# Kernel tuning notes

Measured on AMD Instinct MI355X. Metric: run time of the kernel, lower is better.

Reference implementation:

```python
import jax, jax.numpy as jnp
import numpy as np

N = 8_000_000
NUM_MOLS = 200_000

def setup_inputs() -> dict:
    key = jax.random.key(0)
    k1, k2 = jax.random.split(key)
    atoms_x = jax.random.normal(k1, (N, 3), dtype=jnp.float32)
    graph_batch = jnp.sort(jax.random.randint(k2, (N,), 0, NUM_MOLS, dtype=jnp.int64))
    return {"atoms_x": atoms_x, "graph_batch": graph_batch, "num_mols": NUM_MOLS}

def reference(atoms_x, graph_batch, num_mols):
    # Per-molecule mean via single-pass segment reduction (replaces O(N*num_mols) mask loop)
    seg_sum = jax.ops.segment_sum(atoms_x, graph_batch, num_segments=num_mols)          # [M, 3]
    counts = jax.ops.segment_sum(jnp.ones((atoms_x.shape[0],), atoms_x.dtype),
                                 graph_batch, num_segments=num_mols)                    # [M]
    mean = seg_sum / jnp.maximum(counts, 1.0)[:, None]                                  # empty mols -> 0 center
    return atoms_x - mean[graph_batch]
```

## Files before the change

kernel.cpp:

```cpp
#include <hip/hip_runtime.h>


static constexpr int WAVE   = 64;
static constexpr int WPB    = 4;
static constexpr int TPB    = WAVE * WPB;
static constexpr int CPT    = 16;
static constexpr int WCHUNK = WAVE * CPT;
static constexpr int BCHUNK = WCHUNK * WPB;
static constexpr int SLOTS  = 128;

#define LDS_FENCE() asm volatile("s_waitcnt lgkmcnt(0)" ::: "memory")

__global__ __launch_bounds__(TPB) void fused_center_kernel(
    const float* __restrict__ x, const int* __restrict__ gb,
    float* __restrict__ out, int n) {
  __shared__ float sums_all[WPB][SLOTS * 4];

  const int w = threadIdx.x >> 6;
  const int lane = threadIdx.x & 63;
  float* sums = sums_all[w];

  const long long cs = (long long)blockIdx.x * BCHUNK + (long long)w * WCHUNK;
  if (cs >= (long long)n) return;
  const long long ce = (cs + WCHUNK < (long long)n) ? cs + WCHUNK : (long long)n;
  const int fid = gb[cs];
  const int lid = gb[ce - 1];
  const int span = lid - fid + 1;

  if (span > SLOTS) {
    if (lane == 0) {
      long long i = cs;
      while (i < ce) {
        int id = gb[i];
        long long rs = i; while (rs > 0 && gb[rs - 1] == id) --rs;
        long long re = i; while (re < n && gb[re] == id) ++re;
        float sx = 0.f, sy = 0.f, sz = 0.f;
        for (long long k = rs; k < re; ++k) {
          sx += x[k * 3 + 0]; sy += x[k * 3 + 1]; sz += x[k * 3 + 2];
        }
        float inv = 1.f / (float)(re - rs);
        float mx = sx * inv, my = sy * inv, mz = sz * inv;
        long long we = (re < ce) ? re : ce;
        for (long long k = i; k < we; ++k) {
          out[k * 3 + 0] = x[k * 3 + 0] - mx;
          out[k * 3 + 1] = x[k * 3 + 1] - my;
          out[k * 3 + 2] = x[k * 3 + 2] - mz;
        }
        i = we;
      }
    }
    return;
  }

  const long long base = cs + (long long)lane * CPT;
  const bool full = (base + CPT <= ce);

  float f[CPT * 3];
  int ids[CPT];
  if (full) {
    const float4* xv = reinterpret_cast<const float4*>(x + base * 3);
#pragma unroll
    for (int j = 0; j < CPT * 3 / 4; ++j) {
      float4 v = xv[j];
      f[j * 4 + 0] = v.x; f[j * 4 + 1] = v.y;
      f[j * 4 + 2] = v.z; f[j * 4 + 3] = v.w;
    }
    const int4* gv = reinterpret_cast<const int4*>(gb + base);
#pragma unroll
    for (int j = 0; j < CPT / 4; ++j) {
      int4 g = gv[j];
      ids[j * 4 + 0] = g.x; ids[j * 4 + 1] = g.y;
      ids[j * 4 + 2] = g.z; ids[j * 4 + 3] = g.w;
    }
  }

  for (int i = lane; i < span * 4; i += WAVE) sums[i] = 0.f;
  LDS_FENCE();

  if (full) {
    int cur = ids[0];
    float sx = 0.f, sy = 0.f, sz = 0.f, sc = 0.f;
#pragma unroll
    for (int j = 0; j < CPT; ++j) {
      if (ids[j] != cur) {
        int s = (cur - fid) * 4;
        atomicAdd(&sums[s + 0], sx); atomicAdd(&sums[s + 1], sy);
        atomicAdd(&sums[s + 2], sz); atomicAdd(&sums[s + 3], sc);
        cur = ids[j]; sx = sy = sz = sc = 0.f;
      }
      sx += f[j * 3 + 0]; sy += f[j * 3 + 1]; sz += f[j * 3 + 2]; sc += 1.f;
    }
    {
      int s = (cur - fid) * 4;
      atomicAdd(&sums[s + 0], sx); atomicAdd(&sums[s + 1], sy);
      atomicAdd(&sums[s + 2], sz); atomicAdd(&sums[s + 3], sc);
    }
  } else if (base < ce) {
    for (long long i = base; i < ce; ++i) {
      int s = (gb[i] - fid) * 4;
      atomicAdd(&sums[s + 0], x[i * 3 + 0]);
      atomicAdd(&sums[s + 1], x[i * 3 + 1]);
      atomicAdd(&sums[s + 2], x[i * 3 + 2]);
      atomicAdd(&sums[s + 3], 1.f);
    }
  }

  if (cs > 0) {
    float hx = 0.f, hy = 0.f, hz = 0.f, hc = 0.f;
    long long off = 1 + lane;
    for (;;) {
      long long i = cs - off;
      bool m = (i >= 0) && (gb[i] == fid);
      if (m) {
        hx += x[i * 3 + 0]; hy += x[i * 3 + 1]; hz += x[i * 3 + 2]; hc += 1.f;
      }
      if (__popcll(__ballot(m)) < WAVE) break;
      off += WAVE;
    }
#pragma unroll
    for (int d = 1; d < 64; d <<= 1) {
      hx += __shfl_xor(hx, d); hy += __shfl_xor(hy, d);
      hz += __shfl_xor(hz, d); hc += __shfl_xor(hc, d);
    }
    if (lane == 0 && hc > 0.f) {
      atomicAdd(&sums[0], hx); atomicAdd(&sums[1], hy);
      atomicAdd(&sums[2], hz); atomicAdd(&sums[3], hc);
    }
  }
  if (ce < (long long)n) {
    float hx = 0.f, hy = 0.f, hz = 0.f, hc = 0.f;
    long long off = (long long)lane;
    for (;;) {
      long long i = ce + off;
      bool m = (i < (long long)n) && (gb[i] == lid);
      if (m) {
        hx += x[i * 3 + 0]; hy += x[i * 3 + 1]; hz += x[i * 3 + 2]; hc += 1.f;
      }
      if (__popcll(__ballot(m)) < WAVE) break;
      off += WAVE;
    }
#pragma unroll
    for (int d = 1; d < 64; d <<= 1) {
      hx += __shfl_xor(hx, d); hy += __shfl_xor(hy, d);
      hz += __shfl_xor(hz, d); hc += __shfl_xor(hc, d);
    }
    if (lane == 0 && hc > 0.f) {
      int s = (lid - fid) * 4;
      atomicAdd(&sums[s + 0], hx); atomicAdd(&sums[s + 1], hy);
      atomicAdd(&sums[s + 2], hz); atomicAdd(&sums[s + 3], hc);
    }
  }
  LDS_FENCE();

  for (int s = lane; s < span; s += WAVE) {
    float c = sums[s * 4 + 3];
    if (c > 0.f) {
      float inv = 1.f / c;
      sums[s * 4 + 0] *= inv; sums[s * 4 + 1] *= inv; sums[s * 4 + 2] *= inv;
    }
  }
  LDS_FENCE();

  if (full) {
#pragma unroll
    for (int j = 0; j < CPT; ++j) {
      int s = (ids[j] - fid) * 4;
      f[j * 3 + 0] -= sums[s + 0];
      f[j * 3 + 1] -= sums[s + 1];
      f[j * 3 + 2] -= sums[s + 2];
    }
    float4* ov = reinterpret_cast<float4*>(out + base * 3);
#pragma unroll
    for (int j = 0; j < CPT * 3 / 4; ++j)
      ov[j] = make_float4(f[j * 4 + 0], f[j * 4 + 1],
                          f[j * 4 + 2], f[j * 4 + 3]);
  } else if (base < ce) {
    for (long long i = base; i < ce; ++i) {
      int s = (gb[i] - fid) * 4;
      out[i * 3 + 0] = x[i * 3 + 0] - sums[s + 0];
      out[i * 3 + 1] = x[i * 3 + 1] - sums[s + 1];
      out[i * 3 + 2] = x[i * 3 + 2] - sums[s + 2];
    }
  }
}

extern "C" void kernel_launch(void* const* d_in, const int* in_sizes, int n_in,
                              void* d_out, int out_size, void* d_ws, size_t ws_size,
                              hipStream_t stream) {
  const float* x = (const float*)d_in[0];
  const int* gb = (const int*)d_in[1];
  float* out = (float*)d_out;
  const int n = in_sizes[0] / 3;

  int blocks = (int)(((long long)n + BCHUNK - 1) / BCHUNK);
  fused_center_kernel<<<blocks, TPB, 0, stream>>>(x, gb, out, n);
}
```

Before: 53.22 us.

## Process two chunks per wave with both chunks' loads issued up front

Each wave now handles two consecutive chunks of 12 atoms per lane. It issues the global loads for both chunks before processing the first, so memory latency for the second chunk overlaps with the first chunk's reduction and write-back. Other changes: fid/lid come from register shuffles instead of extra global loads, LDS is zeroed with float4 stores across fixed slots, and the slot count shrinks to 96. The cost is higher register pressure from the two 48-float buffers, which could lower occupancy.

New measurement: 61.47 us. +15.5%, slower.

```diff
diff --git a/kernel.cpp b/kernel.cpp
--- a/kernel.cpp
+++ b/kernel.cpp
@@ -4,27 +4,56 @@
 static constexpr int WAVE   = 64;
 static constexpr int WPB    = 4;
 static constexpr int TPB    = WAVE * WPB;
-static constexpr int CPT    = 16;
+static constexpr int CPT    = 12;
 static constexpr int WCHUNK = WAVE * CPT;
-static constexpr int BCHUNK = WCHUNK * WPB;
-static constexpr int SLOTS  = 128;
+static constexpr int ITERS  = 2;
+static constexpr int SLOTS  = 96;
 
 #define LDS_FENCE() asm volatile("s_waitcnt lgkmcnt(0)" ::: "memory")
 
-__global__ __launch_bounds__(TPB) void fused_center_kernel(
+__device__ __forceinline__ void issue_loads(
     const float* __restrict__ x, const int* __restrict__ gb,
-    float* __restrict__ out, int n) {
-  __shared__ float sums_all[WPB][SLOTS * 4];
-
-  const int w = threadIdx.x >> 6;
-  const int lane = threadIdx.x & 63;
-  float* sums = sums_all[w];
-
-  const long long cs = (long long)blockIdx.x * BCHUNK + (long long)w * WCHUNK;
-  if (cs >= (long long)n) return;
-  const long long ce = (cs + WCHUNK < (long long)n) ? cs + WCHUNK : (long long)n;
-  const int fid = gb[cs];
-  const int lid = gb[ce - 1];
+    long long cs, long long ce, int lane,
+    float* f, int* ids, bool& full) {
+  long long base = cs + (long long)lane * CPT;
+  full = (base + CPT <= ce);
+  if (full) {
+    const float4* xv = reinterpret_cast<const float4*>(x + base * 3);
+#pragma unroll
+    for (int j = 0; j < CPT * 3 / 4; ++j) {
+      float4 v = xv[j];
+      f[j * 4 + 0] = v.x; f[j * 4 + 1] = v.y;
+      f[j * 4 + 2] = v.z; f[j * 4 + 3] = v.w;
+    }
+    const int4* gv = reinterpret_cast<const int4*>(gb + base);
+#pragma unroll
+    for (int j = 0; j < CPT / 4; ++j) {
+      int4 g = gv[j];
+      ids[j * 4 + 0] = g.x; ids[j * 4 + 1] = g.y;
+      ids[j * 4 + 2] = g.z; ids[j * 4 + 3] = g.w;
+    }
+  }
+}
+
+__device__ __forceinline__ void process_chunk(
+    const float* __restrict__ x, const int* __restrict__ gb,
+    float* __restrict__ out, int n, long long cs, long long ce,
+    int lane, float* __restrict__ sums,
+    float* f, int* ids, bool full) {
+  LDS_FENCE();
+  {
+    float4* s4 = reinterpret_cast<float4*>(sums);
+    float4 z = make_float4(0.f, 0.f, 0.f, 0.f);
+#pragma unroll
+    for (int i = 0; i < (SLOTS + WAVE - 1) / WAVE; ++i) {
+      int s = i * WAVE + lane;
+      if (s < SLOTS) s4[s] = z;
+    }
+  }
+
+  const bool partial = (ce - cs) < WCHUNK;
+  const int fid = partial ? gb[cs] : __shfl(ids[0], 0);
+  const int lid = partial ? gb[ce - 1] : __shfl(ids[CPT - 1], WAVE - 1);
   const int span = lid - fid + 1;
 
   if (span > SLOTS) {
@@ -53,29 +82,6 @@
   }
 
   const long long base = cs + (long long)lane * CPT;
-  const bool full = (base + CPT <= ce);
-
-  float f[CPT * 3];
-  int ids[CPT];
-  if (full) {
-    const float4* xv = reinterpret_cast<const float4*>(x + base * 3);
-#pragma unroll
-    for (int j = 0; j < CPT * 3 / 4; ++j) {
-      float4 v = xv[j];
-      f[j * 4 + 0] = v.x; f[j * 4 + 1] = v.y;
-      f[j * 4 + 2] = v.z; f[j * 4 + 3] = v.w;
-    }
-    const int4* gv = reinterpret_cast<const int4*>(gb + base);
-#pragma unroll
-    for (int j = 0; j < CPT / 4; ++j) {
-      int4 g = gv[j];
-      ids[j * 4 + 0] = g.x; ids[j * 4 + 1] = g.y;
-      ids[j * 4 + 2] = g.z; ids[j * 4 + 3] = g.w;
-    }
-  }
-
-  for (int i = lane; i < span * 4; i += WAVE) sums[i] = 0.f;
-  LDS_FENCE();
 
   if (full) {
     int cur = ids[0];
@@ -184,6 +190,37 @@
   }
 }
 
+__global__ __launch_bounds__(TPB) void fused_center_kernel(
+    const float* __restrict__ x, const int* __restrict__ gb,
+    float* __restrict__ out, int n, int nchunks) {
+  __shared__ float sums_all[WPB][SLOTS * 4];
+
+  const int w = threadIdx.x >> 6;
+  const int lane = threadIdx.x & 63;
+  float* sums = sums_all[w];
+
+  const long long g = (long long)blockIdx.x * WPB + w;
+  const long long c0 = g * ITERS;
+  const long long c1 = c0 + 1;
+  if (c0 >= nchunks) return;
+
+  const long long cs0 = c0 * WCHUNK;
+  const long long ce0 = (cs0 + WCHUNK < (long long)n) ? cs0 + WCHUNK : (long long)n;
+  const bool hasB = (c1 < nchunks);
+  const long long cs1 = c1 * WCHUNK;
+  const long long ce1 = (cs1 + WCHUNK < (long long)n) ? cs1 + WCHUNK : (long long)n;
+
+  float fA[CPT * 3]; int idsA[CPT]; bool fullA = false;
+  float fB[CPT * 3]; int idsB[CPT]; bool fullB = false;
+
+  issue_loads(x, gb, cs0, ce0, lane, fA, idsA, fullA);
+  if (hasB) issue_loads(x, gb, cs1, ce1, lane, fB, idsB, fullB);
+
+  process_chunk(x, gb, out, n, cs0, ce0, lane, sums, fA, idsA, fullA);
+  if (hasB)
+    process_chunk(x, gb, out, n, cs1, ce1, lane, sums, fB, idsB, fullB);
+}
+
 extern "C" void kernel_launch(void* const* d_in, const int* in_sizes, int n_in,
                               void* d_out, int out_size, void* d_ws, size_t ws_size,
                               hipStream_t stream) {
@@ -192,6 +229,8 @@
   float* out = (float*)d_out;
   const int n = in_sizes[0] / 3;
 
-  int blocks = (int)(((long long)n + BCHUNK - 1) / BCHUNK);
-  fused_center_kernel<<<blocks, TPB, 0, stream>>>(x, gb, out, n);
-}
+  int nchunks = (int)(((long long)n + WCHUNK - 1) / WCHUNK);
+  long long nwaves = (nchunks + ITERS - 1) / ITERS;
+  int blocks = (int)((nwaves + WPB - 1) / WPB);
+  fused_center_kernel<<<blocks, TPB, 0, stream>>>(x, gb, out, n, nchunks);
+}
```

## Coalesce global loads through padded LDS staging with single-wave blocks

Applied to the files above, without the earlier changes.

Switches each lane from loading its own contiguous strided chunk to coalesced float4/int4 loads across the wave. The data is staged in padded LDS buffers so each lane can then read its own 8 consecutive atoms for segmented accumulation. The output is written back coalesced, with each element's molecule id found by a multiply-shift divide-by-3. Blocks shrink to one wave with 8 atoms per thread and fewer LDS slots, and the tail chunk and fallback are split into separate paths. The aim is better memory coalescing and occupancy, at the cost of extra LDS traffic and index math.

Result: slower. 60.97 us (+14.6%).

```diff
diff --git a/kernel.cpp b/kernel.cpp
--- a/kernel.cpp
+++ b/kernel.cpp
@@ -2,107 +2,172 @@
 
 
 static constexpr int WAVE   = 64;
-static constexpr int WPB    = 4;
-static constexpr int TPB    = WAVE * WPB;
-static constexpr int CPT    = 16;
+static constexpr int TPB    = 64;
+static constexpr int CPT    = 8;
 static constexpr int WCHUNK = WAVE * CPT;
-static constexpr int BCHUNK = WCHUNK * WPB;
-static constexpr int SLOTS  = 128;
+static constexpr int SLOTS  = 96;
+static constexpr int NGRP   = WCHUNK / 16;
+static constexpr int XGRP   = 216;
+static constexpr int IGRP   = 72;
 
 #define LDS_FENCE() asm volatile("s_waitcnt lgkmcnt(0)" ::: "memory")
+
+__device__ void serial_fallback(const float* __restrict__ x,
+                                const int* __restrict__ gb,
+                                float* __restrict__ out, int n,
+                                long long cs, long long ce, int lane) {
+  if (lane != 0) return;
+  long long i = cs;
+  while (i < ce) {
+    int id = gb[i];
+    long long rs = i; while (rs > 0 && gb[rs - 1] == id) --rs;
+    long long re = i; while (re < n && gb[re] == id) ++re;
+    float sx = 0.f, sy = 0.f, sz = 0.f;
+    for (long long k = rs; k < re; ++k) {
+      sx += x[k * 3 + 0]; sy += x[k * 3 + 1]; sz += x[k * 3 + 2];
+    }
+    float inv = 1.f / (float)(re - rs);
+    float mx = sx * inv, my = sy * inv, mz = sz * inv;
+    long long we = (re < ce) ? re : ce;
+    for (long long k = i; k < we; ++k) {
+      out[k * 3 + 0] = x[k * 3 + 0] - mx;
+      out[k * 3 + 1] = x[k * 3 + 1] - my;
+      out[k * 3 + 2] = x[k * 3 + 2] - mz;
+    }
+    i = we;
+  }
+}
 
 __global__ __launch_bounds__(TPB) void fused_center_kernel(
     const float* __restrict__ x, const int* __restrict__ gb,
     float* __restrict__ out, int n) {
-  __shared__ float sums_all[WPB][SLOTS * 4];
-
-  const int w = threadIdx.x >> 6;
-  const int lane = threadIdx.x & 63;
-  float* sums = sums_all[w];
-
-  const long long cs = (long long)blockIdx.x * BCHUNK + (long long)w * WCHUNK;
-  if (cs >= (long long)n) return;
+  __shared__ alignas(16) char xbuf[NGRP * XGRP];
+  __shared__ alignas(16) char ibuf[NGRP * IGRP];
+  __shared__ alignas(16) float sums[SLOTS * 4];
+
+  const int lane = threadIdx.x;
+  const long long cs = (long long)blockIdx.x * WCHUNK;
   const long long ce = (cs + WCHUNK < (long long)n) ? cs + WCHUNK : (long long)n;
-  const int fid = gb[cs];
-  const int lid = gb[ce - 1];
-  const int span = lid - fid + 1;
-
-  if (span > SLOTS) {
-    if (lane == 0) {
-      long long i = cs;
-      while (i < ce) {
-        int id = gb[i];
-        long long rs = i; while (rs > 0 && gb[rs - 1] == id) --rs;
-        long long re = i; while (re < n && gb[re] == id) ++re;
-        float sx = 0.f, sy = 0.f, sz = 0.f;
-        for (long long k = rs; k < re; ++k) {
-          sx += x[k * 3 + 0]; sy += x[k * 3 + 1]; sz += x[k * 3 + 2];
-        }
-        float inv = 1.f / (float)(re - rs);
-        float mx = sx * inv, my = sy * inv, mz = sz * inv;
-        long long we = (re < ce) ? re : ce;
-        for (long long k = i; k < we; ++k) {
-          out[k * 3 + 0] = x[k * 3 + 0] - mx;
-          out[k * 3 + 1] = x[k * 3 + 1] - my;
-          out[k * 3 + 2] = x[k * 3 + 2] - mz;
-        }
-        i = we;
-      }
-    }
-    return;
-  }
-
-  const long long base = cs + (long long)lane * CPT;
-  const bool full = (base + CPT <= ce);
-
-  float f[CPT * 3];
-  int ids[CPT];
-  if (full) {
-    const float4* xv = reinterpret_cast<const float4*>(x + base * 3);
-#pragma unroll
-    for (int j = 0; j < CPT * 3 / 4; ++j) {
-      float4 v = xv[j];
-      f[j * 4 + 0] = v.x; f[j * 4 + 1] = v.y;
-      f[j * 4 + 2] = v.z; f[j * 4 + 3] = v.w;
-    }
-    const int4* gv = reinterpret_cast<const int4*>(gb + base);
-#pragma unroll
-    for (int j = 0; j < CPT / 4; ++j) {
-      int4 g = gv[j];
-      ids[j * 4 + 0] = g.x; ids[j * 4 + 1] = g.y;
-      ids[j * 4 + 2] = g.z; ids[j * 4 + 3] = g.w;
-    }
-  }
-
-  for (int i = lane; i < span * 4; i += WAVE) sums[i] = 0.f;
-  LDS_FENCE();
-
-  if (full) {
-    int cur = ids[0];
-    float sx = 0.f, sy = 0.f, sz = 0.f, sc = 0.f;
-#pragma unroll
-    for (int j = 0; j < CPT; ++j) {
-      if (ids[j] != cur) {
-        int s = (cur - fid) * 4;
-        atomicAdd(&sums[s + 0], sx); atomicAdd(&sums[s + 1], sy);
-        atomicAdd(&sums[s + 2], sz); atomicAdd(&sums[s + 3], sc);
-        cur = ids[j]; sx = sy = sz = sc = 0.f;
-      }
-      sx += f[j * 3 + 0]; sy += f[j * 3 + 1]; sz += f[j * 3 + 2]; sc += 1.f;
-    }
-    {
-      int s = (cur - fid) * 4;
-      atomicAdd(&sums[s + 0], sx); atomicAdd(&sums[s + 1], sy);
-      atomicAdd(&sums[s + 2], sz); atomicAdd(&sums[s + 3], sc);
-    }
-  } else if (base < ce) {
-    for (long long i = base; i < ce; ++i) {
+
+  if (ce - cs < WCHUNK) {
+    const int fid = gb[cs];
+    const int lid = gb[ce - 1];
+    const int span = lid - fid + 1;
+    if (span > SLOTS) { serial_fallback(x, gb, out, n, cs, ce, lane); return; }
+    for (int s = lane; s < span * 4; s += WAVE) sums[s] = 0.f;
+    LDS_FENCE();
+    for (long long i = cs + lane; i < ce; i += WAVE) {
       int s = (gb[i] - fid) * 4;
       atomicAdd(&sums[s + 0], x[i * 3 + 0]);
       atomicAdd(&sums[s + 1], x[i * 3 + 1]);
       atomicAdd(&sums[s + 2], x[i * 3 + 2]);
       atomicAdd(&sums[s + 3], 1.f);
     }
+    if (cs > 0) {
+      float hx = 0.f, hy = 0.f, hz = 0.f, hc = 0.f;
+      long long off = 1 + lane;
+      for (;;) {
+        long long i = cs - off;
+        bool m = (i >= 0) && (gb[i] == fid);
+        if (m) { hx += x[i*3+0]; hy += x[i*3+1]; hz += x[i*3+2]; hc += 1.f; }
+        if (__popcll(__ballot(m)) < WAVE) break;
+        off += WAVE;
+      }
+#pragma unroll
+      for (int d = 1; d < 64; d <<= 1) {
+        hx += __shfl_xor(hx, d); hy += __shfl_xor(hy, d);
+        hz += __shfl_xor(hz, d); hc += __shfl_xor(hc, d);
+      }
+      if (lane == 0 && hc > 0.f) {
+        atomicAdd(&sums[0], hx); atomicAdd(&sums[1], hy);
+        atomicAdd(&sums[2], hz); atomicAdd(&sums[3], hc);
+      }
+    }
+    LDS_FENCE();
+    for (int s = lane; s < span; s += WAVE) {
+      float c = sums[s * 4 + 3];
+      if (c > 0.f) {
+        float inv = 1.f / c;
+        sums[s*4+0] *= inv; sums[s*4+1] *= inv; sums[s*4+2] *= inv;
+      }
+    }
+    LDS_FENCE();
+    for (long long i = cs + lane; i < ce; i += WAVE) {
+      int s = (gb[i] - fid) * 4;
+      out[i * 3 + 0] = x[i * 3 + 0] - sums[s + 0];
+      out[i * 3 + 1] = x[i * 3 + 1] - sums[s + 1];
+      out[i * 3 + 2] = x[i * 3 + 2] - sums[s + 2];
+    }
+    return;
+  }
+
+  float4 xr[6];
+  const float4* xv = reinterpret_cast<const float4*>(x + cs * 3);
+#pragma unroll
+  for (int j = 0; j < 6; ++j) xr[j] = xv[j * WAVE + lane];
+  int4 gr[2];
+  const int4* gv = reinterpret_cast<const int4*>(gb + cs);
+#pragma unroll
+  for (int j = 0; j < 2; ++j) gr[j] = gv[j * WAVE + lane];
+
+#pragma unroll
+  for (int j = 0; j < 6; ++j) {
+    int i = j * WAVE + lane;
+    int k0 = 2 * i, k1 = 2 * i + 1;
+    *reinterpret_cast<float2*>(xbuf + (k0 / 24) * XGRP + (k0 % 24) * 8) =
+        make_float2(xr[j].x, xr[j].y);
+    *reinterpret_cast<float2*>(xbuf + (k1 / 24) * XGRP + (k1 % 24) * 8) =
+        make_float2(xr[j].z, xr[j].w);
+  }
+#pragma unroll
+  for (int j = 0; j < 2; ++j) {
+    int i = j * WAVE + lane;
+    int k0 = 2 * i, k1 = 2 * i + 1;
+    *reinterpret_cast<int2*>(ibuf + (k0 / 8) * IGRP + (k0 % 8) * 8) =
+        make_int2(gr[j].x, gr[j].y);
+    *reinterpret_cast<int2*>(ibuf + (k1 / 8) * IGRP + (k1 % 8) * 8) =
+        make_int2(gr[j].z, gr[j].w);
+  }
+  {
+    float4 z = make_float4(0.f, 0.f, 0.f, 0.f);
+    reinterpret_cast<float4*>(sums)[lane] = z;
+    if (lane < SLOTS - WAVE) reinterpret_cast<float4*>(sums)[WAVE + lane] = z;
+  }
+  LDS_FENCE();
+
+  int idk[CPT];
+  const int a0 = lane * CPT;
+#pragma unroll
+  for (int j = 0; j < CPT; ++j) {
+    int a = a0 + j;
+    idk[j] = *reinterpret_cast<const int*>(ibuf + (a / 16) * IGRP + (a % 16) * 4);
+  }
+  const int fid = __shfl(idk[0], 0);
+  const int lid = __shfl(idk[CPT - 1], WAVE - 1);
+  const int span = lid - fid + 1;
+  if (span > SLOTS) { serial_fallback(x, gb, out, n, cs, ce, lane); return; }
+
+  {
+    int cur = idk[0];
+    float sx = 0.f, sy = 0.f, sz = 0.f, sc = 0.f;
+#pragma unroll
+    for (int j = 0; j < CPT; ++j) {
+      if (idk[j] != cur) {
+        int s = (cur - fid) * 4;
+        atomicAdd(&sums[s + 0], sx); atomicAdd(&sums[s + 1], sy);
+        atomicAdd(&sums[s + 2], sz); atomicAdd(&sums[s + 3], sc);
+        cur = idk[j]; sx = sy = sz = sc = 0.f;
+      }
+      int a = a0 + j;
+      const char* p = xbuf + (a / 16) * XGRP + (a % 16) * 12;
+      sx += *reinterpret_cast<const float*>(p + 0);
+      sy += *reinterpret_cast<const float*>(p + 4);
+      sz += *reinterpret_cast<const float*>(p + 8);
+      sc += 1.f;
+    }
+    int s = (cur - fid) * 4;
+    atomicAdd(&sums[s + 0], sx); atomicAdd(&sums[s + 1], sy);
+    atomicAdd(&sums[s + 2], sz); atomicAdd(&sums[s + 3], sc);
   }
 
   if (cs > 0) {
@@ -111,9 +176,7 @@
     for (;;) {
       long long i = cs - off;
       bool m = (i >= 0) && (gb[i] == fid);
-      if (m) {
-        hx += x[i * 3 + 0]; hy += x[i * 3 + 1]; hz += x[i * 3 + 2]; hc += 1.f;
-      }
+      if (m) { hx += x[i*3+0]; hy += x[i*3+1]; hz += x[i*3+2]; hc += 1.f; }
       if (__popcll(__ballot(m)) < WAVE) break;
       off += WAVE;
     }
@@ -133,9 +196,7 @@
     for (;;) {
       long long i = ce + off;
       bool m = (i < (long long)n) && (gb[i] == lid);
-      if (m) {
-        hx += x[i * 3 + 0]; hy += x[i * 3 + 1]; hz += x[i * 3 + 2]; hc += 1.f;
-      }
+      if (m) { hx += x[i*3+0]; hy += x[i*3+1]; hz += x[i*3+2]; hc += 1.f; }
       if (__popcll(__ballot(m)) < WAVE) break;
       off += WAVE;
     }
@@ -156,31 +217,33 @@
     float c = sums[s * 4 + 3];
     if (c > 0.f) {
       float inv = 1.f / c;
-      sums[s * 4 + 0] *= inv; sums[s * 4 + 1] *= inv; sums[s * 4 + 2] *= inv;
+      sums[s*4+0] *= inv; sums[s*4+1] *= inv; sums[s*4+2] *= inv;
     }
   }
   LDS_FENCE();
 
-  if (full) {
-#pragma unroll
-    for (int j = 0; j < CPT; ++j) {
-      int s = (ids[j] - fid) * 4;
-      f[j * 3 + 0] -= sums[s + 0];
-      f[j * 3 + 1] -= sums[s + 1];
-      f[j * 3 + 2] -= sums[s + 2];
-    }
-    float4* ov = reinterpret_cast<float4*>(out + base * 3);
-#pragma unroll
-    for (int j = 0; j < CPT * 3 / 4; ++j)
-      ov[j] = make_float4(f[j * 4 + 0], f[j * 4 + 1],
-                          f[j * 4 + 2], f[j * 4 + 3]);
-  } else if (base < ce) {
-    for (long long i = base; i < ce; ++i) {
-      int s = (gb[i] - fid) * 4;
-      out[i * 3 + 0] = x[i * 3 + 0] - sums[s + 0];
-      out[i * 3 + 1] = x[i * 3 + 1] - sums[s + 1];
-      out[i * 3 + 2] = x[i * 3 + 2] - sums[s + 2];
-    }
+  float4* ov = reinterpret_cast<float4*>(out + cs * 3);
+#pragma unroll
+  for (int j = 0; j < 6; ++j) {
+    int i = j * WAVE + lane;
+    int e = 4 * i;
+    float4 o;
+#pragma unroll
+    for (int c = 0; c < 4; ++c) {
+      int ee = e + c;
+      int atom = (int)(((unsigned)ee * 0xAAABu) >> 17);
+      int comp = ee - atom * 3;
+      int id = *reinterpret_cast<const int*>(
+          ibuf + (atom / 16) * IGRP + (atom % 16) * 4);
+      float m = sums[(id - fid) * 4 + comp];
+      float v = (c == 0) ? xr[j].x : (c == 1) ? xr[j].y
+              : (c == 2) ? xr[j].z : xr[j].w;
+      if (c == 0) o.x = v - m;
+      else if (c == 1) o.y = v - m;
+      else if (c == 2) o.z = v - m;
+      else o.w = v - m;
+    }
+    ov[i] = o;
   }
 }
 
@@ -192,6 +255,6 @@
   float* out = (float*)d_out;
   const int n = in_sizes[0] / 3;
 
-  int blocks = (int)(((long long)n + BCHUNK - 1) / BCHUNK);
+  int blocks = (int)(((long long)n + WCHUNK - 1) / WCHUNK);
   fused_center_kernel<<<blocks, TPB, 0, stream>>>(x, gb, out, n);
 }
```

## Split into interior-sum kernel and edge-fixup kernel using global per-molecule workspace

Applied to the files above, without the earlier changes.

Replaces the per-wave halo scans (which walked backward and forward past chunk boundaries to complete edge molecules) with a two-kernel scheme. The first kernel writes interior molecule sums to a global workspace, atomically adds boundary molecule partials, and finishes centering for interior atoms. The second kernel reads the completed sums and writes output for the first and last molecule of each chunk. This trades the redundant halo reads for a memset, a second launch, global atomics and an extra re-read of boundary atoms. The workspace size is hardcoded to 200000 molecules.

Result: slower. 87.70 us (+64.8%).

```diff
diff --git a/kernel.cpp b/kernel.cpp
--- a/kernel.cpp
+++ b/kernel.cpp
@@ -6,25 +6,57 @@
 static constexpr int TPB    = WAVE * WPB;
 static constexpr int CPT    = 16;
 static constexpr int WCHUNK = WAVE * CPT;
-static constexpr int BCHUNK = WCHUNK * WPB;
 static constexpr int SLOTS  = 128;
+static constexpr int M_MOLS = 200000;
 
 #define LDS_FENCE() asm volatile("s_waitcnt lgkmcnt(0)" ::: "memory")
 
-__global__ __launch_bounds__(TPB) void fused_center_kernel(
+__global__ __launch_bounds__(TPB) void k1_sum_interior(
     const float* __restrict__ x, const int* __restrict__ gb,
-    float* __restrict__ out, int n) {
+    float* __restrict__ ws, float* __restrict__ out, int n) {
   __shared__ float sums_all[WPB][SLOTS * 4];
 
   const int w = threadIdx.x >> 6;
   const int lane = threadIdx.x & 63;
   float* sums = sums_all[w];
 
-  const long long cs = (long long)blockIdx.x * BCHUNK + (long long)w * WCHUNK;
+  const long long cs = ((long long)blockIdx.x * WPB + w) * WCHUNK;
   if (cs >= (long long)n) return;
   const long long ce = (cs + WCHUNK < (long long)n) ? cs + WCHUNK : (long long)n;
-  const int fid = gb[cs];
-  const int lid = gb[ce - 1];
+
+  if (ce - cs < WCHUNK) {
+    for (long long i = cs + lane; i < ce; i += WAVE) {
+      int id = gb[i];
+      atomicAdd(&ws[(size_t)id * 4 + 0], x[i * 3 + 0]);
+      atomicAdd(&ws[(size_t)id * 4 + 1], x[i * 3 + 1]);
+      atomicAdd(&ws[(size_t)id * 4 + 2], x[i * 3 + 2]);
+      atomicAdd(&ws[(size_t)id * 4 + 3], 1.f);
+    }
+    return;
+  }
+
+  const long long base = cs + (long long)lane * CPT;
+
+  float f[CPT * 3];
+  int ids[CPT];
+  {
+    const float4* xv = reinterpret_cast<const float4*>(x + base * 3);
+#pragma unroll
+    for (int j = 0; j < CPT * 3 / 4; ++j) {
+      float4 v = xv[j];
+      f[j * 4 + 0] = v.x; f[j * 4 + 1] = v.y;
+      f[j * 4 + 2] = v.z; f[j * 4 + 3] = v.w;
+    }
+    const int4* gv = reinterpret_cast<const int4*>(gb + base);
+#pragma unroll
+    for (int j = 0; j < CPT / 4; ++j) {
+      int4 g = gv[j];
+      ids[j * 4 + 0] = g.x; ids[j * 4 + 1] = g.y;
+      ids[j * 4 + 2] = g.z; ids[j * 4 + 3] = g.w;
+    }
+  }
+  const int fid = __shfl(ids[0], 0);
+  const int lid = __shfl(ids[CPT - 1], WAVE - 1);
   const int span = lid - fid + 1;
 
   if (span > SLOTS) {
@@ -32,52 +64,35 @@
       long long i = cs;
       while (i < ce) {
         int id = gb[i];
-        long long rs = i; while (rs > 0 && gb[rs - 1] == id) --rs;
-        long long re = i; while (re < n && gb[re] == id) ++re;
+        long long re = i;
         float sx = 0.f, sy = 0.f, sz = 0.f;
-        for (long long k = rs; k < re; ++k) {
-          sx += x[k * 3 + 0]; sy += x[k * 3 + 1]; sz += x[k * 3 + 2];
+        while (re < ce && gb[re] == id) {
+          sx += x[re*3+0]; sy += x[re*3+1]; sz += x[re*3+2]; ++re;
         }
-        float inv = 1.f / (float)(re - rs);
-        float mx = sx * inv, my = sy * inv, mz = sz * inv;
-        long long we = (re < ce) ? re : ce;
-        for (long long k = i; k < we; ++k) {
-          out[k * 3 + 0] = x[k * 3 + 0] - mx;
-          out[k * 3 + 1] = x[k * 3 + 1] - my;
-          out[k * 3 + 2] = x[k * 3 + 2] - mz;
+        float cnt = (float)(re - i);
+        atomicAdd(&ws[(size_t)id*4+0], sx);
+        atomicAdd(&ws[(size_t)id*4+1], sy);
+        atomicAdd(&ws[(size_t)id*4+2], sz);
+        atomicAdd(&ws[(size_t)id*4+3], cnt);
+        if (id != fid && id != lid) {
+          float inv = 1.f / cnt;
+          float mx = sx*inv, my = sy*inv, mz = sz*inv;
+          for (long long k = i; k < re; ++k) {
+            out[k*3+0] = x[k*3+0] - mx;
+            out[k*3+1] = x[k*3+1] - my;
+            out[k*3+2] = x[k*3+2] - mz;
+          }
         }
-        i = we;
+        i = re;
       }
     }
     return;
-  }
-
-  const long long base = cs + (long long)lane * CPT;
-  const bool full = (base + CPT <= ce);
-
-  float f[CPT * 3];
-  int ids[CPT];
-  if (full) {
-    const float4* xv = reinterpret_cast<const float4*>(x + base * 3);
-#pragma unroll
-    for (int j = 0; j < CPT * 3 / 4; ++j) {
-      float4 v = xv[j];
-      f[j * 4 + 0] = v.x; f[j * 4 + 1] = v.y;
-      f[j * 4 + 2] = v.z; f[j * 4 + 3] = v.w;
-    }
-    const int4* gv = reinterpret_cast<const int4*>(gb + base);
-#pragma unroll
-    for (int j = 0; j < CPT / 4; ++j) {
-      int4 g = gv[j];
-      ids[j * 4 + 0] = g.x; ids[j * 4 + 1] = g.y;
-      ids[j * 4 + 2] = g.z; ids[j * 4 + 3] = g.w;
-    }
   }
 
   for (int i = lane; i < span * 4; i += WAVE) sums[i] = 0.f;
   LDS_FENCE();
 
-  if (full) {
+  {
     int cur = ids[0];
     float sx = 0.f, sy = 0.f, sz = 0.f, sc = 0.f;
 #pragma unroll
@@ -90,78 +105,35 @@
       }
       sx += f[j * 3 + 0]; sy += f[j * 3 + 1]; sz += f[j * 3 + 2]; sc += 1.f;
     }
-    {
-      int s = (cur - fid) * 4;
-      atomicAdd(&sums[s + 0], sx); atomicAdd(&sums[s + 1], sy);
-      atomicAdd(&sums[s + 2], sz); atomicAdd(&sums[s + 3], sc);
-    }
-  } else if (base < ce) {
-    for (long long i = base; i < ce; ++i) {
-      int s = (gb[i] - fid) * 4;
-      atomicAdd(&sums[s + 0], x[i * 3 + 0]);
-      atomicAdd(&sums[s + 1], x[i * 3 + 1]);
-      atomicAdd(&sums[s + 2], x[i * 3 + 2]);
-      atomicAdd(&sums[s + 3], 1.f);
-    }
-  }
-
-  if (cs > 0) {
-    float hx = 0.f, hy = 0.f, hz = 0.f, hc = 0.f;
-    long long off = 1 + lane;
-    for (;;) {
-      long long i = cs - off;
-      bool m = (i >= 0) && (gb[i] == fid);
-      if (m) {
-        hx += x[i * 3 + 0]; hy += x[i * 3 + 1]; hz += x[i * 3 + 2]; hc += 1.f;
-      }
-      if (__popcll(__ballot(m)) < WAVE) break;
-      off += WAVE;
-    }
-#pragma unroll
-    for (int d = 1; d < 64; d <<= 1) {
-      hx += __shfl_xor(hx, d); hy += __shfl_xor(hy, d);
-      hz += __shfl_xor(hz, d); hc += __shfl_xor(hc, d);
-    }
-    if (lane == 0 && hc > 0.f) {
-      atomicAdd(&sums[0], hx); atomicAdd(&sums[1], hy);
-      atomicAdd(&sums[2], hz); atomicAdd(&sums[3], hc);
-    }
-  }
-  if (ce < (long long)n) {
-    float hx = 0.f, hy = 0.f, hz = 0.f, hc = 0.f;
-    long long off = (long long)lane;
-    for (;;) {
-      long long i = ce + off;
-      bool m = (i < (long long)n) && (gb[i] == lid);
-      if (m) {
-        hx += x[i * 3 + 0]; hy += x[i * 3 + 1]; hz += x[i * 3 + 2]; hc += 1.f;
-      }
-      if (__popcll(__ballot(m)) < WAVE) break;
-      off += WAVE;
-    }
-#pragma unroll
-    for (int d = 1; d < 64; d <<= 1) {
-      hx += __shfl_xor(hx, d); hy += __shfl_xor(hy, d);
-      hz += __shfl_xor(hz, d); hc += __shfl_xor(hc, d);
-    }
-    if (lane == 0 && hc > 0.f) {
-      int s = (lid - fid) * 4;
-      atomicAdd(&sums[s + 0], hx); atomicAdd(&sums[s + 1], hy);
-      atomicAdd(&sums[s + 2], hz); atomicAdd(&sums[s + 3], hc);
-    }
+    int s = (cur - fid) * 4;
+    atomicAdd(&sums[s + 0], sx); atomicAdd(&sums[s + 1], sy);
+    atomicAdd(&sums[s + 2], sz); atomicAdd(&sums[s + 3], sc);
   }
   LDS_FENCE();
 
   for (int s = lane; s < span; s += WAVE) {
-    float c = sums[s * 4 + 3];
-    if (c > 0.f) {
-      float inv = 1.f / c;
-      sums[s * 4 + 0] *= inv; sums[s * 4 + 1] *= inv; sums[s * 4 + 2] *= inv;
+    float4 v = *reinterpret_cast<float4*>(&sums[s * 4]);
+    size_t mol = (size_t)(fid + s) * 4;
+    if (s == 0 || s == span - 1) {
+      atomicAdd(&ws[mol + 0], v.x); atomicAdd(&ws[mol + 1], v.y);
+      atomicAdd(&ws[mol + 2], v.z); atomicAdd(&ws[mol + 3], v.w);
+    } else {
+      *reinterpret_cast<float4*>(&ws[mol]) = v;
+    }
+  }
+
+  for (int s = lane; s < span; s += WAVE) {
+    if (s > 0 && s < span - 1) {
+      float c = sums[s * 4 + 3];
+      if (c > 0.f) {
+        float inv = 1.f / c;
+        sums[s*4+0] *= inv; sums[s*4+1] *= inv; sums[s*4+2] *= inv;
+      }
     }
   }
   LDS_FENCE();
 
-  if (full) {
+  if (ids[0] != fid && ids[CPT - 1] != lid) {
 #pragma unroll
     for (int j = 0; j < CPT; ++j) {
       int s = (ids[j] - fid) * 4;
@@ -174,12 +146,76 @@
     for (int j = 0; j < CPT * 3 / 4; ++j)
       ov[j] = make_float4(f[j * 4 + 0], f[j * 4 + 1],
                           f[j * 4 + 2], f[j * 4 + 3]);
-  } else if (base < ce) {
-    for (long long i = base; i < ce; ++i) {
-      int s = (gb[i] - fid) * 4;
-      out[i * 3 + 0] = x[i * 3 + 0] - sums[s + 0];
-      out[i * 3 + 1] = x[i * 3 + 1] - sums[s + 1];
-      out[i * 3 + 2] = x[i * 3 + 2] - sums[s + 2];
+  } else {
+#pragma unroll
+    for (int j = 0; j < CPT; ++j) {
+      int id = ids[j];
+      if (id != fid && id != lid) {
+        int s = (id - fid) * 4;
+        long long i = base + j;
+        out[i * 3 + 0] = f[j * 3 + 0] - sums[s + 0];
+        out[i * 3 + 1] = f[j * 3 + 1] - sums[s + 1];
+        out[i * 3 + 2] = f[j * 3 + 2] - sums[s + 2];
+      }
+    }
+  }
+}
+
+__global__ __launch_bounds__(TPB) void k2_edges(
+    const float* __restrict__ x, const int* __restrict__ gb,
+    const float* __restrict__ ws, float* __restrict__ out, int n) {
+  const int w = threadIdx.x >> 6;
+  const int lane = threadIdx.x & 63;
+
+  const long long cs = ((long long)blockIdx.x * WPB + w) * WCHUNK;
+  if (cs >= (long long)n) return;
+  const long long ce = (cs + WCHUNK < (long long)n) ? cs + WCHUNK : (long long)n;
+
+  if (ce - cs < WCHUNK) {
+    for (long long i = cs + lane; i < ce; i += WAVE) {
+      int id = gb[i];
+      float4 v = *reinterpret_cast<const float4*>(&ws[(size_t)id * 4]);
+      float inv = 1.f / v.w;
+      out[i * 3 + 0] = x[i * 3 + 0] - v.x * inv;
+      out[i * 3 + 1] = x[i * 3 + 1] - v.y * inv;
+      out[i * 3 + 2] = x[i * 3 + 2] - v.z * inv;
+    }
+    return;
+  }
+
+  const int fid = gb[cs];
+  const int lid = gb[ce - 1];
+
+  {
+    float4 v = *reinterpret_cast<const float4*>(&ws[(size_t)fid * 4]);
+    float inv = 1.f / v.w;
+    float mx = v.x * inv, my = v.y * inv, mz = v.z * inv;
+    long long i = cs + lane;
+    for (;;) {
+      bool m = (i < ce) && (gb[i] == fid);
+      if (m) {
+        out[i * 3 + 0] = x[i * 3 + 0] - mx;
+        out[i * 3 + 1] = x[i * 3 + 1] - my;
+        out[i * 3 + 2] = x[i * 3 + 2] - mz;
+      }
+      if (__popcll(__ballot(m)) < WAVE) break;
+      i += WAVE;
+    }
+  }
+  if (lid != fid) {
+    float4 v = *reinterpret_cast<const float4*>(&ws[(size_t)lid * 4]);
+    float inv = 1.f / v.w;
+    float mx = v.x * inv, my = v.y * inv, mz = v.z * inv;
+    long long i = ce - 1 - lane;
+    for (;;) {
+      bool m = (i >= cs) && (gb[i] == lid);
+      if (m) {
+        out[i * 3 + 0] = x[i * 3 + 0] - mx;
+        out[i * 3 + 1] = x[i * 3 + 1] - my;
+        out[i * 3 + 2] = x[i * 3 + 2] - mz;
+      }
+      if (__popcll(__ballot(m)) < WAVE) break;
+      i -= WAVE;
     }
   }
 }
@@ -190,8 +226,13 @@
   const float* x = (const float*)d_in[0];
   const int* gb = (const int*)d_in[1];
   float* out = (float*)d_out;
+  float* ws = (float*)d_ws;
   const int n = in_sizes[0] / 3;
 
-  int blocks = (int)(((long long)n + BCHUNK - 1) / BCHUNK);
-  fused_center_kernel<<<blocks, TPB, 0, stream>>>(x, gb, out, n);
+  hipMemsetAsync(ws, 0, (size_t)M_MOLS * 4 * sizeof(float), stream);
+
+  long long nchunks = ((long long)n + WCHUNK - 1) / WCHUNK;
+  int blocks = (int)((nchunks + WPB - 1) / WPB);
+  k1_sum_interior<<<blocks, TPB, 0, stream>>>(x, gb, ws, out, n);
+  k2_edges<<<blocks, TPB, 0, stream>>>(x, gb, ws, out, n);
 }
```
